# Optimization experiments

Hardware: AMD Instinct MI355X
Metric: run time of the kernel (lower is better)

The kernel has to match this reference:

```python
import jax, jax.numpy as jnp
import numpy as np

B, S, D = 2, 1024, 4096
N_HEADS, KV_HEADS, HEAD_DIM = 32, 8, 128
EPS = 1e-6
ROPE_THETA = 1e6


def setup_inputs() -> dict:
    key = jax.random.key(0)
    ks = jax.random.split(key, 7)
    scale = 0.02
    x = jax.random.normal(ks[0], (B, S, D), dtype=jnp.float32)
    positions = jnp.broadcast_to(jnp.arange(S, dtype=jnp.int32)[None, :], (B, S))
    wq = jax.random.normal(ks[1], (D, N_HEADS, HEAD_DIM), dtype=jnp.float32) * scale
    wk = jax.random.normal(ks[2], (D, KV_HEADS, HEAD_DIM), dtype=jnp.float32) * scale
    wv = jax.random.normal(ks[3], (D, KV_HEADS, HEAD_DIM), dtype=jnp.float32) * scale
    wo = jax.random.normal(ks[4], (N_HEADS, HEAD_DIM, D), dtype=jnp.float32) * scale
    q_norm_w = 1.0 + jax.random.normal(ks[5], (HEAD_DIM,), dtype=jnp.float32) * 0.01
    k_norm_w = 1.0 + jax.random.normal(ks[6], (HEAD_DIM,), dtype=jnp.float32) * 0.01
    return {"x": x, "positions": positions, "wq": wq, "wk": wk, "wv": wv,
            "wo": wo, "q_norm_w": q_norm_w, "k_norm_w": k_norm_w}


def _rms_norm(t, w):
    # per-head RMSNorm over last (head_dim) axis
    var = jnp.mean(jnp.square(t), axis=-1, keepdims=True)
    return (t * jax.lax.rsqrt(var + EPS)) * w


def _rope(t, positions):
    # neox-style rotary embedding; t: [B, S, n, H], positions: [B, S]
    half = t.shape[-1] // 2
    inv_freq = 1.0 / (ROPE_THETA ** (jnp.arange(0, half, dtype=jnp.float32) / half))
    ang = positions.astype(jnp.float32)[..., None] * inv_freq  # [B, S, half]
    cos = jnp.cos(ang)[:, :, None, :]  # [B, S, 1, half]
    sin = jnp.sin(ang)[:, :, None, :]
    t1, t2 = t[..., :half], t[..., half:]
    return jnp.concatenate([t1 * cos - t2 * sin, t2 * cos + t1 * sin], axis=-1)


def reference(x, positions, wq, wk, wv, wo, q_norm_w, k_norm_w):
    # QKV projections (einsum layers: 'bsd,dnh->bsnh')
    q = jnp.einsum('bsd,dnh->bsnh', x, wq)  # [B, S, N, H]
    k = jnp.einsum('bsd,dkh->bskh', x, wk)  # [B, S, K, H]
    v = jnp.einsum('bsd,dkh->bskh', x, wv)
    # per-head QK RMSNorm, then RoPE
    q = _rope(_rms_norm(q, q_norm_w), positions)
    k = _rope(_rms_norm(k, k_norm_w), positions)
    # GQA: expand KV heads to query heads
    groups = N_HEADS // KV_HEADS
    k = jnp.repeat(k, groups, axis=2)  # [B, S, N, H]
    v = jnp.repeat(v, groups, axis=2)
    sm_scale = HEAD_DIM ** -0.5
    scores = jnp.einsum('bqnh,btnh->bnqt', q, k) * sm_scale  # [B, N, S, S]
    causal = jnp.tril(jnp.ones((S, S), dtype=bool))
    scores = jnp.where(causal[None, None], scores, jnp.finfo(scores.dtype).min)
    probs = jax.nn.softmax(scores, axis=-1)
    attn = jnp.einsum('bnqt,btnh->bqnh', probs, v)  # [B, S, N, H]
    out = jnp.einsum('bqnh,nhd->bqd', attn, wo)  # output projection
    return out
```

## Files before the change

kernel.cpp:

```cpp
#include <hip/hip_runtime.h>
#include <stdint.h>

#define S_LEN   1024
#define D_MODEL 4096
#define NHQ     32
#define NKV     8
#define HD      128
#define NTOK    2048
#define NQKV    6144
#define SM_SCALE 0.08838834764831843f
#define LOG2E    1.4426950408889634f

typedef __attribute__((ext_vector_type(8))) __bf16 bf16x8;
typedef __attribute__((ext_vector_type(4))) float f32x4;

__device__ __forceinline__ unsigned short f2bf(float f) {
  union { float f; unsigned u; } x; x.f = f;
  unsigned r = x.u + 0x7fffu + ((x.u >> 16) & 1u);
  return (unsigned short)(r >> 16);
}
__device__ __forceinline__ float bf2f(unsigned short u) {
  union { unsigned u; float f; } x; x.u = (unsigned)u << 16; return x.f;
}

__device__ __forceinline__ void gload_lds16(const void* g, void* l) {
  __builtin_amdgcn_global_load_lds((__attribute__((address_space(1))) void*)g,
                                   (__attribute__((address_space(3))) void*)l,
                                   16, 0, 0);
}

__global__ void k_f32_to_bf16(const float* __restrict__ in,
                              unsigned short* __restrict__ out, int n8) {
  int i = blockIdx.x * blockDim.x + threadIdx.x;
  if (i >= n8) return;
  const float4* p = (const float4*)(in + (size_t)i * 8);
  float4 v0 = p[0], v1 = p[1];
  uint4 o;
  o.x = f2bf(v0.x) | ((unsigned)f2bf(v0.y) << 16);
  o.y = f2bf(v0.z) | ((unsigned)f2bf(v0.w) << 16);
  o.z = f2bf(v1.x) | ((unsigned)f2bf(v1.y) << 16);
  o.w = f2bf(v1.z) | ((unsigned)f2bf(v1.w) << 16);
  *(uint4*)(out + (size_t)i * 8) = o;
}

__global__ void k_transpose(const float* __restrict__ in,
                            unsigned short* __restrict__ out, int R, int C) {
  __shared__ float t[32][33];
  int c = threadIdx.x & 31, r0 = threadIdx.x >> 5;
  int cb = blockIdx.x * 32, rb = blockIdx.y * 32;
#pragma unroll
  for (int i = 0; i < 4; ++i) {
    int r = r0 + i * 8;
    t[r][c] = in[(size_t)(rb + r) * C + cb + c];
  }
  __syncthreads();
#pragma unroll
  for (int i = 0; i < 4; ++i) {
    int r = r0 + i * 8;
    out[(size_t)(cb + r) * R + rb + c] = f2bf(t[c][r]);
  }
}


#define LGKM0 { asm volatile("s_waitcnt lgkmcnt(0)" ::: "memory"); \
                __builtin_amdgcn_sched_barrier(0); }
#define BAR   __builtin_amdgcn_s_barrier();
#define GATE  { if constexpr (NF == 4)                                          \
                  asm volatile("s_waitcnt vmcnt(8)" ::: "memory");              \
                else                                                            \
                  asm volatile("s_waitcnt vmcnt(6)" ::: "memory"); }

#define STGA(h, bufb, kOff)                                                     \
  _Pragma("unroll")                                                             \
  for (int i_ = 0; i_ < 2; ++i_)                                                \
    gload_lds16(gA[i_] + (kOff) + (h) * 64,                                     \
                smem + (bufb) + (h) * 16384 + dA[i_]);

#define STGB(h, bufb, kOff)                                                     \
  _Pragma("unroll")                                                             \
  for (int i_ = 0; i_ < NF / 2; ++i_)                                           \
    gload_lds16(gB[i_] + (kOff) + (h) * 64,                                     \
                smem + (bufb) + 32768 + (h) * (NF * 4096) + dB[i_]);

#define RD_A8(dst, kh, bufb)                                                    \
  _Pragma("unroll")                                                             \
  for (int f = 0; f < 8; ++f) {                                                 \
    int row = wr * 128 + f * 16 + lr;                                           \
    dst[f] = *(const bf16x8*)(smem + (bufb) + (kh) * 16384 + row * 64           \
                              + ((lg * 16) ^ (((row >> 1) & 3) << 4)));         \
  }

#define RD_B(dst, kh, bufb)                                                     \
  _Pragma("unroll")                                                             \
  for (int nf = 0; nf < NF; ++nf) {                                             \
    int row = wc * (NF * 16) + nf * 16 + lr;                                    \
    dst[nf] = *(const bf16x8*)(smem + (bufb) + 32768 + (kh) * (NF * 4096)       \
                               + row * 64 + ((lg * 16) ^ (((row >> 1) & 3) << 4))); \
  }

#define MFMA32(AF, BF)                                                          \
  __builtin_amdgcn_s_setprio(1);                                                \
  _Pragma("unroll")                                                             \
  for (int f = 0; f < 8; ++f)                                                   \
    _Pragma("unroll")                                                           \
    for (int nf = 0; nf < NF; ++nf)                                             \
      acc[f][nf] = __builtin_amdgcn_mfma_f32_16x16x32_bf16(                     \
          AF[f], BF[nf], acc[f][nf], 0, 0, 0);                                  \
  __builtin_amdgcn_s_setprio(0);

template <int NF, typename OutT>
__global__ __launch_bounds__(512, 1) void k_gemmfl(
    const unsigned short* __restrict__ Aptr,
    const unsigned short* __restrict__ Bptr,
    OutT* __restrict__ C,
    int Kstride, int ldc, int NT, int SGN, int nxn) {
  extern __shared__ __align__(16) char smem[];
  constexpr int BUFST = 32768 + NF * 8192;
  int tid = threadIdx.x;
  int l = tid & 63;
  int w = tid >> 6;
  int lr = l & 15, lg = l >> 4;
  int wr = w >> 2, wc = w & 3;
  int per_xcd = gridDim.x >> 3;
  int x8 = blockIdx.x & 7, i = blockIdx.x >> 3;
  int SGM = per_xcd / SGN;
  int xr = x8 / nxn, xc = x8 - xr * nxn;
  int iy = i / SGN;
  int by = xr * SGM + iy, bx = xc * SGN + (i - iy * SGN);
  int bm = by * 256, bn = bx * (NF * 64);

  const char* gA[2]; int dA[2];
#pragma unroll
  for (int i_ = 0; i_ < 2; ++i_) {
    int lin = i_ * 512 + tid;
    int r_ = lin >> 2, slot = lin & 3, sw = slot ^ ((r_ >> 1) & 3);
    gA[i_] = (const char*)(Aptr + (size_t)(bm + r_) * Kstride) + sw * 16;
    dA[i_] = lin * 16;
  }
  const char* gB[NF / 2]; int dB[NF / 2];
#pragma unroll
  for (int i_ = 0; i_ < NF / 2; ++i_) {
    int lin = i_ * 512 + tid;
    int r_ = lin >> 2, slot = lin & 3, sw = slot ^ ((r_ >> 1) & 3);
    gB[i_] = (const char*)(Bptr + (size_t)(bn + r_) * Kstride) + sw * 16;
    dB[i_] = lin * 16;
  }

  f32x4 acc[8][NF] = {};
  bf16x8 af[8], bf[NF];

  STGA(0, 0, 0) STGB(0, 0, 0)
  STGA(1, 0, 0) STGB(1, 0, 0)
  STGA(0, BUFST, 128) STGB(0, BUFST, 128)
  STGA(1, BUFST, 128) STGB(1, BUFST, 128)

  for (int kt = 0; kt < NT; ++kt) {
    int curb = (kt & 1) * BUFST;
    int kcl = (kt + 2 < NT) ? kt + 2 : NT - 1;
    int kOff = kcl * 128;
    GATE
    BAR
    RD_A8(af, 0, curb) RD_B(bf, 0, curb)
    LGKM0
    BAR
    STGA(0, curb, kOff) STGB(0, curb, kOff)
    MFMA32(af, bf)
    RD_A8(af, 1, curb) RD_B(bf, 1, curb)
    LGKM0
    BAR
    STGA(1, curb, kOff) STGB(1, curb, kOff)
    MFMA32(af, bf)
  }

#pragma unroll
  for (int f = 0; f < 8; ++f)
#pragma unroll
    for (int nf = 0; nf < NF; ++nf)
#pragma unroll
      for (int j = 0; j < 4; ++j) {
        size_t idx = (size_t)(bm + wr * 128 + f * 16 + lg * 4 + j) * ldc +
                     bn + wc * (NF * 16) + nf * 16 + lr;
        float v = acc[f][nf][j];
        if constexpr (sizeof(OutT) == 2) C[idx] = f2bf(v);
        else C[idx] = v;
      }
}

__global__ void k_norm_rope(const unsigned short* __restrict__ qkv,
                            const float* __restrict__ w,
                            const int* __restrict__ positions,
                            unsigned short* __restrict__ out, int nheads, int colbase,
                            float oscale) {
  int wid = blockIdx.x * 4 + (threadIdx.x >> 6);
  int lane = threadIdx.x & 63;
  int token = wid / nheads, head = wid - token * nheads;
  const unsigned short* src = qkv + (size_t)token * NQKV + colbase + head * HD;
  float e0 = bf2f(src[lane]), e1 = bf2f(src[lane + 64]);
  float ss = e0 * e0 + e1 * e1;
#pragma unroll
  for (int m = 1; m < 64; m <<= 1) ss += __shfl_xor(ss, m, 64);
  float rs = rsqrtf(ss * (1.0f / 128.0f) + 1e-6f);
  float n0 = e0 * rs * w[lane], n1 = e1 * rs * w[lane + 64];
  int pos = positions[token];
  float invf = exp2f((float)lane * (-19.931568569324174f / 64.0f));
  float ang = (float)pos * invf;
  float sv, cv;
  sincosf(ang, &sv, &cv);
  float o0 = (n0 * cv - n1 * sv) * oscale;
  float o1 = (n1 * cv + n0 * sv) * oscale;
  int b = token >> 10, s = token & 1023;
  size_t ob = ((size_t)(b * nheads + head) * S_LEN + s) * HD;
  out[ob + lane] = f2bf(o0);
  out[ob + 64 + lane] = f2bf(o1);
}

__global__ void k_v_transpose(const unsigned short* __restrict__ qkv,
                              unsigned short* __restrict__ vt) {
  __shared__ unsigned short t[32][33];
  int slice = blockIdx.z;
  int b = slice >> 3, kh = slice & 7;
  const unsigned short* in = qkv + (size_t)(b * S_LEN) * NQKV + 5120 + kh * HD;
  unsigned short* out = vt + (size_t)slice * HD * S_LEN;
  int c = threadIdx.x & 31, r0 = threadIdx.x >> 5;
  int s0 = blockIdx.y * 32, d0 = blockIdx.x * 32;
#pragma unroll
  for (int i = 0; i < 4; ++i) {
    int r = r0 + i * 8;
    t[r][c] = in[(size_t)(s0 + r) * NQKV + d0 + c];
  }
  __syncthreads();
#pragma unroll
  for (int i = 0; i < 4; ++i) {
    int r = r0 + i * 8;
    out[(size_t)(d0 + r) * S_LEN + s0 + c] = t[c][r];
  }
}

__global__ __launch_bounds__(512) void k_attn(const unsigned short* __restrict__ qh,
                                              const unsigned short* __restrict__ kbuf,
                                              const unsigned short* __restrict__ vtbuf,
                                              unsigned short* __restrict__ attn_out) {
  __shared__ __align__(16) unsigned short k_lds[64 * 128];
  __shared__ __align__(16) unsigned short v_lds[128 * 64];
  __shared__ __align__(16) unsigned short p_lds[8][16 * 64];
  int b = blockIdx.z, h = blockIdx.y, bx = blockIdx.x;
  int khd = h >> 2;
  int tid = threadIdx.x, w = tid >> 6, l = tid & 63;
  int lr = l & 15, lg = l >> 4;
  const unsigned short* K = kbuf + (size_t)(b * NKV + khd) * S_LEN * HD;
  const unsigned short* VT = vtbuf + (size_t)(b * NKV + khd) * HD * S_LEN;
  char* klp = (char*)k_lds;
  char* vlp = (char*)v_lds;
  char* plp = (char*)p_lds[w];
  int swz = (lr & 7) << 4;

  for (int strip = 0; strip < 2; ++strip) {
    int qs = strip ? (7 - bx) : bx;
    int q0 = qs * 128;
    int rbase = q0 + w * 16;
    const unsigned short* Q = qh + ((size_t)(b * NHQ + h) * S_LEN + rbase) * HD;
    bf16x8 qf[4];
#pragma unroll
    for (int kk = 0; kk < 4; ++kk)
      qf[kk] = *(const bf16x8*)&Q[(size_t)lr * HD + kk * 32 + lg * 8];

    f32x4 o[8] = {};
    float m_[4], l_[4];
#pragma unroll
    for (int j = 0; j < 4; ++j) { m_[j] = -1e30f; l_[j] = 0.0f; }

    int nt = 2 * qs + 2;
    for (int t = 0; t < nt; ++t) {
      int t0 = t * 64;
      __syncthreads();
#pragma unroll
      for (int it = 0; it < 2; ++it) {
        int db = (tid + it * 512) * 16;
        int kr = db >> 8, kc = db & 255;
        gload_lds16(K + (size_t)(t0 + kr) * HD + ((kc ^ ((kr & 7) << 4)) >> 1), klp + db);
        int vr = db >> 7, vc = db & 127;
        gload_lds16(VT + (size_t)vr * S_LEN + t0 + ((vc ^ ((vr & 7) << 4)) >> 1), vlp + db);
      }
      __syncthreads();

      f32x4 sc[4];
      __builtin_amdgcn_s_setprio(1);
#pragma unroll
      for (int ct = 0; ct < 4; ++ct) {
        f32x4 s = {};
        int row = ct * 16 + lr;
#pragma unroll
        for (int kk = 0; kk < 4; ++kk) {
          bf16x8 kf = *(const bf16x8*)(klp + row * 256 + ((kk * 64 + lg * 16) ^ swz));
          s = __builtin_amdgcn_mfma_f32_16x16x32_bf16(qf[kk], kf, s, 0, 0, 0);
        }
        sc[ct] = s;
      }
      __builtin_amdgcn_s_setprio(0);

      bool fullw = (t0 + 63 <= rbase);
      float alpha[4];
#pragma unroll
      for (int j = 0; j < 4; ++j) {
        if (!fullw) {
          int rg = rbase + lg * 4 + j;
#pragma unroll
          for (int ct = 0; ct < 4; ++ct)
            sc[ct][j] = (t0 + ct * 16 + lr <= rg) ? sc[ct][j] : -1e30f;
        }
        float mx = fmaxf(fmaxf(sc[0][j], sc[1][j]), fmaxf(sc[2][j], sc[3][j]));
#pragma unroll
        for (int msk = 1; msk < 16; msk <<= 1) mx = fmaxf(mx, __shfl_xor(mx, msk, 64));
        float mn = fmaxf(m_[j], mx);
        alpha[j] = exp2f(m_[j] - mn);
        int q = lg * 4 + j;
        int psw = (q & 7) << 4;
        float ps = 0.0f;
#pragma unroll
        for (int ct = 0; ct < 4; ++ct) {
          float p = exp2f(sc[ct][j] - mn);
          ps += p;
          *(unsigned short*)(plp + q * 128 + (((ct * 16 + lr) * 2) ^ psw)) = f2bf(p);
        }
#pragma unroll
        for (int msk = 1; msk < 16; msk <<= 1) ps += __shfl_xor(ps, msk, 64);
        l_[j] = l_[j] * alpha[j] + ps;
        m_[j] = mn;
      }
#pragma unroll
      for (int dc = 0; dc < 8; ++dc) {
        o[dc][0] *= alpha[0]; o[dc][1] *= alpha[1];
        o[dc][2] *= alpha[2]; o[dc][3] *= alpha[3];
      }
      asm volatile("s_waitcnt lgkmcnt(0)" ::: "memory");
      __builtin_amdgcn_s_setprio(1);
#pragma unroll
      for (int kt = 0; kt < 2; ++kt) {
        bf16x8 pa = *(const bf16x8*)(plp + lr * 128 + ((kt * 64 + lg * 16) ^ swz));
#pragma unroll
        for (int dc = 0; dc < 8; ++dc) {
          int vrow = dc * 16 + lr;
          bf16x8 vf = *(const bf16x8*)(vlp + vrow * 128 + ((kt * 64 + lg * 16) ^ swz));
          o[dc] = __builtin_amdgcn_mfma_f32_16x16x32_bf16(pa, vf, o[dc], 0, 0, 0);
        }
      }
      __builtin_amdgcn_s_setprio(0);
    }

#pragma unroll
    for (int j = 0; j < 4; ++j) {
      int rg = rbase + lg * 4 + j;
      size_t row = (size_t)(b * S_LEN + rg) * D_MODEL + h * HD;
      float inv = 1.0f / l_[j];
#pragma unroll
      for (int dc = 0; dc < 8; ++dc)
        attn_out[row + dc * 16 + lr] = f2bf(o[dc][j] * inv);
    }
  }
}

extern "C" void kernel_launch(void* const* d_in, const int* in_sizes, int n_in,
                              void* d_out, int out_size, void* d_ws, size_t ws_size,
                              hipStream_t stream) {
  const float* x        = (const float*)d_in[0];
  const int* positions  = (const int*)d_in[1];
  const float* wq       = (const float*)d_in[2];
  const float* wk       = (const float*)d_in[3];
  const float* wv       = (const float*)d_in[4];
  const float* wo       = (const float*)d_in[5];
  const float* qnw      = (const float*)d_in[6];
  const float* knw      = (const float*)d_in[7];
  float* out            = (float*)d_out;

  char* ws = (char*)d_ws;
  unsigned short* xb   = (unsigned short*)(ws);
  unsigned short* wB   = (unsigned short*)(ws + 16777216);
  unsigned short* woT  = (unsigned short*)(ws + 67108864);
  unsigned short* qkvb = (unsigned short*)(ws + 100663296);
  unsigned short* qh   = wB;
  unsigned short* khb  = (unsigned short*)(ws + 33554432);
  unsigned short* vtb  = (unsigned short*)(ws + 37748736);
  unsigned short* attn = xb;

  dim3 tb(256);
  k_f32_to_bf16<<<4096, tb, 0, stream>>>(x, xb, 1048576);
  k_transpose<<<dim3(128, 128), tb, 0, stream>>>(wq, wB, 4096, 4096);
  k_transpose<<<dim3(32, 128), tb, 0, stream>>>(wk, wB + (size_t)4096 * 4096, 4096, 1024);
  k_transpose<<<dim3(32, 128), tb, 0, stream>>>(wv, wB + (size_t)5120 * 4096, 4096, 1024);
  k_transpose<<<dim3(128, 128), tb, 0, stream>>>(wo, woT, 4096, 4096);

  k_gemmfl<4, unsigned short><<<dim3(192), dim3(512), 131072, stream>>>(
      xb, wB, qkvb, 4096, 6144, 64, 6, 4);

  k_norm_rope<<<16384, tb, 0, stream>>>(qkvb, qnw, positions, qh, 32, 0, SM_SCALE * LOG2E);
  k_norm_rope<<<4096, tb, 0, stream>>>(qkvb, knw, positions, khb, 8, 4096, 1.0f);
  k_v_transpose<<<dim3(4, 32, 16), tb, 0, stream>>>(qkvb, vtb);

  k_attn<<<dim3(4, 32, 2), dim3(512), 0, stream>>>(qh, khb, vtb, attn);

  k_gemmfl<2, float><<<dim3(256), dim3(512), 98304, stream>>>(
      attn, woT, out, 4096, 4096, 64, 8, 4);
}
```

Before: 329.1 us.

## Replace large-tile GEMMs with 128x128 double-buffered GEMM, vectorize transposes, fuse norm-rope

The 256-row, 512-thread GEMM with a deep prefetch pipeline is replaced by a simpler 128x128-tile, 256-thread kernel. It uses two LDS buffers over 64-wide K steps and runs more blocks. The weight transpose now uses 64x64 tiles with float4 loads and ushort4 stores, and the Q and K norm+RoPE launches are merged into one kernel. Smaller tiles cut per-block data reuse and add a barrier and a full vmcnt wait on every K step, which may leave the GEMMs less latency-hidden than the tuned pipeline.

```diff
diff --git a/kernel.cpp b/kernel.cpp
--- a/kernel.cpp
+++ b/kernel.cpp
@@ -43,21 +43,29 @@
   *(uint4*)(out + (size_t)i * 8) = o;
 }
 
-__global__ void k_transpose(const float* __restrict__ in,
-                            unsigned short* __restrict__ out, int R, int C) {
-  __shared__ float t[32][33];
-  int c = threadIdx.x & 31, r0 = threadIdx.x >> 5;
-  int cb = blockIdx.x * 32, rb = blockIdx.y * 32;
+__global__ __launch_bounds__(256) void k_transpose64(const float* __restrict__ in,
+                                                     unsigned short* __restrict__ out,
+                                                     int R, int C) {
+  __shared__ float t[64][65];
+  int rb = blockIdx.y * 64, cb = blockIdx.x * 64;
+  int c4 = (threadIdx.x & 15) * 4;
+  int r0 = threadIdx.x >> 4;
 #pragma unroll
   for (int i = 0; i < 4; ++i) {
-    int r = r0 + i * 8;
-    t[r][c] = in[(size_t)(rb + r) * C + cb + c];
+    int r = r0 + i * 16;
+    float4 v = *(const float4*)&in[(size_t)(rb + r) * C + cb + c4];
+    t[r][c4] = v.x; t[r][c4 + 1] = v.y; t[r][c4 + 2] = v.z; t[r][c4 + 3] = v.w;
   }
   __syncthreads();
+  int rg = (threadIdx.x & 15) * 4;
+  int cc0 = threadIdx.x >> 4;
 #pragma unroll
   for (int i = 0; i < 4; ++i) {
-    int r = r0 + i * 8;
-    out[(size_t)(cb + r) * R + rb + c] = f2bf(t[c][r]);
+    int cc = cc0 + i * 16;
+    ushort4 u;
+    u.x = f2bf(t[rg][cc]);     u.y = f2bf(t[rg + 1][cc]);
+    u.z = f2bf(t[rg + 2][cc]); u.w = f2bf(t[rg + 3][cc]);
+    *(ushort4*)&out[(size_t)(cb + cc) * R + rb + rg] = u;
   }
 }
 
@@ -65,136 +73,113 @@
 #define LGKM0 { asm volatile("s_waitcnt lgkmcnt(0)" ::: "memory"); \
                 __builtin_amdgcn_sched_barrier(0); }
 #define BAR   __builtin_amdgcn_s_barrier();
-#define GATE  { if constexpr (NF == 4)                                          \
-                  asm volatile("s_waitcnt vmcnt(8)" ::: "memory");              \
-                else                                                            \
-                  asm volatile("s_waitcnt vmcnt(6)" ::: "memory"); }
-
-#define STGA(h, bufb, kOff)                                                     \
-  _Pragma("unroll")                                                             \
-  for (int i_ = 0; i_ < 2; ++i_)                                                \
-    gload_lds16(gA[i_] + (kOff) + (h) * 64,                                     \
-                smem + (bufb) + (h) * 16384 + dA[i_]);
-
-#define STGB(h, bufb, kOff)                                                     \
-  _Pragma("unroll")                                                             \
-  for (int i_ = 0; i_ < NF / 2; ++i_)                                           \
-    gload_lds16(gB[i_] + (kOff) + (h) * 64,                                     \
-                smem + (bufb) + 32768 + (h) * (NF * 4096) + dB[i_]);
-
-#define RD_A8(dst, kh, bufb)                                                    \
-  _Pragma("unroll")                                                             \
-  for (int f = 0; f < 8; ++f) {                                                 \
-    int row = wr * 128 + f * 16 + lr;                                           \
-    dst[f] = *(const bf16x8*)(smem + (bufb) + (kh) * 16384 + row * 64           \
-                              + ((lg * 16) ^ (((row >> 1) & 3) << 4)));         \
-  }
-
-#define RD_B(dst, kh, bufb)                                                     \
-  _Pragma("unroll")                                                             \
-  for (int nf = 0; nf < NF; ++nf) {                                             \
-    int row = wc * (NF * 16) + nf * 16 + lr;                                    \
-    dst[nf] = *(const bf16x8*)(smem + (bufb) + 32768 + (kh) * (NF * 4096)       \
-                               + row * 64 + ((lg * 16) ^ (((row >> 1) & 3) << 4))); \
-  }
-
-#define MFMA32(AF, BF)                                                          \
-  __builtin_amdgcn_s_setprio(1);                                                \
-  _Pragma("unroll")                                                             \
-  for (int f = 0; f < 8; ++f)                                                   \
-    _Pragma("unroll")                                                           \
-    for (int nf = 0; nf < NF; ++nf)                                             \
-      acc[f][nf] = __builtin_amdgcn_mfma_f32_16x16x32_bf16(                     \
-          AF[f], BF[nf], acc[f][nf], 0, 0, 0);                                  \
-  __builtin_amdgcn_s_setprio(0);
-
-template <int NF, typename OutT>
-__global__ __launch_bounds__(512, 1) void k_gemmfl(
+
+template <typename OutT>
+__global__ __launch_bounds__(256) void k_gemm128(
     const unsigned short* __restrict__ Aptr,
     const unsigned short* __restrict__ Bptr,
     OutT* __restrict__ C,
     int Kstride, int ldc, int NT, int SGN, int nxn) {
-  extern __shared__ __align__(16) char smem[];
-  constexpr int BUFST = 32768 + NF * 8192;
+  __shared__ __align__(16) char smem[2][16384];
   int tid = threadIdx.x;
   int l = tid & 63;
   int w = tid >> 6;
   int lr = l & 15, lg = l >> 4;
-  int wr = w >> 2, wc = w & 3;
+  int wr = w >> 1, wc = w & 1;
   int per_xcd = gridDim.x >> 3;
   int x8 = blockIdx.x & 7, i = blockIdx.x >> 3;
   int SGM = per_xcd / SGN;
   int xr = x8 / nxn, xc = x8 - xr * nxn;
   int iy = i / SGN;
   int by = xr * SGM + iy, bx = xc * SGN + (i - iy * SGN);
-  int bm = by * 256, bn = bx * (NF * 64);
-
-  const char* gA[2]; int dA[2];
+  int bm = by * 128, bn = bx * 128;
+
+  const char* gA[2]; const char* gB[2]; int dA[2], dB[2];
 #pragma unroll
   for (int i_ = 0; i_ < 2; ++i_) {
-    int lin = i_ * 512 + tid;
+    int lin = i_ * 256 + tid;
     int r_ = lin >> 2, slot = lin & 3, sw = slot ^ ((r_ >> 1) & 3);
     gA[i_] = (const char*)(Aptr + (size_t)(bm + r_) * Kstride) + sw * 16;
+    gB[i_] = (const char*)(Bptr + (size_t)(bn + r_) * Kstride) + sw * 16;
     dA[i_] = lin * 16;
-  }
-  const char* gB[NF / 2]; int dB[NF / 2];
-#pragma unroll
-  for (int i_ = 0; i_ < NF / 2; ++i_) {
-    int lin = i_ * 512 + tid;
-    int r_ = lin >> 2, slot = lin & 3, sw = slot ^ ((r_ >> 1) & 3);
-    gB[i_] = (const char*)(Bptr + (size_t)(bn + r_) * Kstride) + sw * 16;
     dB[i_] = lin * 16;
   }
 
-  f32x4 acc[8][NF] = {};
-  bf16x8 af[8], bf[NF];
-
-  STGA(0, 0, 0) STGB(0, 0, 0)
-  STGA(1, 0, 0) STGB(1, 0, 0)
-  STGA(0, BUFST, 128) STGB(0, BUFST, 128)
-  STGA(1, BUFST, 128) STGB(1, BUFST, 128)
+  f32x4 acc[4][4] = {};
+  bf16x8 af[4], bf[4];
+
+#pragma unroll
+  for (int i_ = 0; i_ < 2; ++i_) {
+    gload_lds16(gA[i_], &smem[0][0] + dA[i_]);
+    gload_lds16(gB[i_], &smem[0][8192] + dB[i_]);
+  }
+  asm volatile("s_waitcnt vmcnt(0)" ::: "memory");
+  BAR
 
   for (int kt = 0; kt < NT; ++kt) {
-    int curb = (kt & 1) * BUFST;
-    int kcl = (kt + 2 < NT) ? kt + 2 : NT - 1;
-    int kOff = kcl * 128;
-    GATE
+    int cur = kt & 1;
+    int kcl = (kt + 1 < NT) ? kt + 1 : NT - 1;
+    int kOff = kcl * 64;
+#pragma unroll
+    for (int i_ = 0; i_ < 2; ++i_) {
+      gload_lds16(gA[i_] + kOff, &smem[cur ^ 1][0] + dA[i_]);
+      gload_lds16(gB[i_] + kOff, &smem[cur ^ 1][8192] + dB[i_]);
+    }
+#pragma unroll
+    for (int mf = 0; mf < 4; ++mf) {
+      int row = wr * 64 + mf * 16 + lr;
+      af[mf] = *(const bf16x8*)(&smem[cur][0] + row * 64 +
+                                ((lg * 16) ^ (((row >> 1) & 3) << 4)));
+    }
+#pragma unroll
+    for (int nf = 0; nf < 4; ++nf) {
+      int row = wc * 64 + nf * 16 + lr;
+      bf[nf] = *(const bf16x8*)(&smem[cur][8192] + row * 64 +
+                                ((lg * 16) ^ (((row >> 1) & 3) << 4)));
+    }
+    LGKM0
+    __builtin_amdgcn_s_setprio(1);
+#pragma unroll
+    for (int mf = 0; mf < 4; ++mf)
+#pragma unroll
+      for (int nf = 0; nf < 4; ++nf)
+        acc[mf][nf] = __builtin_amdgcn_mfma_f32_16x16x32_bf16(
+            af[mf], bf[nf], acc[mf][nf], 0, 0, 0);
+    __builtin_amdgcn_s_setprio(0);
+    asm volatile("s_waitcnt vmcnt(0)" ::: "memory");
     BAR
-    RD_A8(af, 0, curb) RD_B(bf, 0, curb)
-    LGKM0
-    BAR
-    STGA(0, curb, kOff) STGB(0, curb, kOff)
-    MFMA32(af, bf)
-    RD_A8(af, 1, curb) RD_B(bf, 1, curb)
-    LGKM0
-    BAR
-    STGA(1, curb, kOff) STGB(1, curb, kOff)
-    MFMA32(af, bf)
-  }
-
-#pragma unroll
-  for (int f = 0; f < 8; ++f)
-#pragma unroll
-    for (int nf = 0; nf < NF; ++nf)
+  }
+
+#pragma unroll
+  for (int mf = 0; mf < 4; ++mf)
+#pragma unroll
+    for (int nf = 0; nf < 4; ++nf)
 #pragma unroll
       for (int j = 0; j < 4; ++j) {
-        size_t idx = (size_t)(bm + wr * 128 + f * 16 + lg * 4 + j) * ldc +
-                     bn + wc * (NF * 16) + nf * 16 + lr;
-        float v = acc[f][nf][j];
+        size_t idx = (size_t)(bm + wr * 64 + mf * 16 + lg * 4 + j) * ldc +
+                     bn + wc * 64 + nf * 16 + lr;
+        float v = acc[mf][nf][j];
         if constexpr (sizeof(OutT) == 2) C[idx] = f2bf(v);
         else C[idx] = v;
       }
 }
 
-__global__ void k_norm_rope(const unsigned short* __restrict__ qkv,
-                            const float* __restrict__ w,
-                            const int* __restrict__ positions,
-                            unsigned short* __restrict__ out, int nheads, int colbase,
-                            float oscale) {
+__global__ void k_norm_rope_qk(const unsigned short* __restrict__ qkv,
+                               const float* __restrict__ qw,
+                               const float* __restrict__ kw,
+                               const int* __restrict__ positions,
+                               unsigned short* __restrict__ qh,
+                               unsigned short* __restrict__ khb,
+                               float qscale) {
   int wid = blockIdx.x * 4 + (threadIdx.x >> 6);
   int lane = threadIdx.x & 63;
-  int token = wid / nheads, head = wid - token * nheads;
-  const unsigned short* src = qkv + (size_t)token * NQKV + colbase + head * HD;
+  int token = wid / 40, hh = wid - token * 40;
+  bool isq = hh < 32;
+  int head = isq ? hh : hh - 32;
+  int colbase = isq ? head * HD : 4096 + head * HD;
+  const float* w = isq ? qw : kw;
+  float oscale = isq ? qscale : 1.0f;
+  const unsigned short* src = qkv + (size_t)token * NQKV + colbase;
   float e0 = bf2f(src[lane]), e1 = bf2f(src[lane + 64]);
   float ss = e0 * e0 + e1 * e1;
 #pragma unroll
@@ -209,9 +194,10 @@
   float o0 = (n0 * cv - n1 * sv) * oscale;
   float o1 = (n1 * cv + n0 * sv) * oscale;
   int b = token >> 10, s = token & 1023;
-  size_t ob = ((size_t)(b * nheads + head) * S_LEN + s) * HD;
-  out[ob + lane] = f2bf(o0);
-  out[ob + 64 + lane] = f2bf(o1);
+  unsigned short* dst = isq ? qh + ((size_t)(b * NHQ + head) * S_LEN + s) * HD
+                            : khb + ((size_t)(b * NKV + head) * S_LEN + s) * HD;
+  dst[lane] = f2bf(o0);
+  dst[64 + lane] = f2bf(o1);
 }
 
 __global__ void k_v_transpose(const unsigned short* __restrict__ qkv,
@@ -384,20 +370,20 @@
 
   dim3 tb(256);
   k_f32_to_bf16<<<4096, tb, 0, stream>>>(x, xb, 1048576);
-  k_transpose<<<dim3(128, 128), tb, 0, stream>>>(wq, wB, 4096, 4096);
-  k_transpose<<<dim3(32, 128), tb, 0, stream>>>(wk, wB + (size_t)4096 * 4096, 4096, 1024);
-  k_transpose<<<dim3(32, 128), tb, 0, stream>>>(wv, wB + (size_t)5120 * 4096, 4096, 1024);
-  k_transpose<<<dim3(128, 128), tb, 0, stream>>>(wo, woT, 4096, 4096);
-
-  k_gemmfl<4, unsigned short><<<dim3(192), dim3(512), 131072, stream>>>(
-      xb, wB, qkvb, 4096, 6144, 64, 6, 4);
-
-  k_norm_rope<<<16384, tb, 0, stream>>>(qkvb, qnw, positions, qh, 32, 0, SM_SCALE * LOG2E);
-  k_norm_rope<<<4096, tb, 0, stream>>>(qkvb, knw, positions, khb, 8, 4096, 1.0f);
+  k_transpose64<<<dim3(64, 64), tb, 0, stream>>>(wq, wB, 4096, 4096);
+  k_transpose64<<<dim3(16, 64), tb, 0, stream>>>(wk, wB + (size_t)4096 * 4096, 4096, 1024);
+  k_transpose64<<<dim3(16, 64), tb, 0, stream>>>(wv, wB + (size_t)5120 * 4096, 4096, 1024);
+  k_transpose64<<<dim3(64, 64), tb, 0, stream>>>(wo, woT, 4096, 4096);
+
+  k_gemm128<unsigned short><<<dim3(768), tb, 0, stream>>>(
+      xb, wB, qkvb, 4096, 6144, 128, 12, 4);
+
+  k_norm_rope_qk<<<20480, tb, 0, stream>>>(qkvb, qnw, knw, positions, qh, khb,
+                                           SM_SCALE * LOG2E);
   k_v_transpose<<<dim3(4, 32, 16), tb, 0, stream>>>(qkvb, vtb);
 
   k_attn<<<dim3(4, 32, 2), dim3(512), 0, stream>>>(qh, khb, vtb, attn);
 
-  k_gemmfl<2, float><<<dim3(256), dim3(512), 98304, stream>>>(
-      attn, woT, out, 4096, 4096, 64, 8, 4);
-}
+  k_gemm128<float><<<dim3(512), tb, 0, stream>>>(
+      attn, woT, out, 4096, 4096, 128, 8, 4);
+}
```

Result: slower. 358.2 us (+8.9%).
